# Optimization experiments

Measured on AMD Instinct MI355X. Metric: run time of the kernel, lower is better.

## Reference

```python
import jax, jax.numpy as jnp
import numpy as np

LAYERS = [2, 1024, 512, 256, 128, 1]
LB = jnp.array([0.0, 0.0], dtype=jnp.float32)
UB = jnp.array([2.0 * np.pi, 1.0], dtype=jnp.float32)


def _block_diag_mask(num_blocks, bs1, bs2):
    return jnp.kron(jnp.eye(num_blocks, dtype=jnp.float32), jnp.ones((bs1, bs2), jnp.float32))


def _masks():
    # masks for l in range(2, num_Layers - 2) with num_Layers = len(LAYERS) = 6 -> l in {2, 3}
    width = [LAYERS[0]] + [(2 ** (i - 1)) * LAYERS[i] for i in range(1, len(LAYERS) - 1)] + [LAYERS[-1]]
    masks = []
    for l in range(2, len(LAYERS) - 2):
        num_blocks = 2 ** (l - 1)
        bs1 = width[l] // num_blocks
        bs2 = 2 * LAYERS[l + 1]
        masks.append(_block_diag_mask(num_blocks, bs1, bs2))
    return masks


def setup_inputs() -> dict:
    key = jax.random.key(0)
    ks = jax.random.split(key, 8)
    N = 65536
    H = 1024

    def xavier(k, fi, fo):
        lim = float(np.sqrt(6.0 / (fi + fo)))
        return jax.random.uniform(k, (fi, fo), jnp.float32, -lim, lim)

    X = jax.random.uniform(ks[0], (N, 2), jnp.float32, 0.0, 1.0) * (UB - LB) + LB
    return {
        "X": X,
        "W0": xavier(ks[1], 2, H), "b0": jnp.zeros((1, H), jnp.float32),
        "W1": xavier(ks[2], H, H), "b1": jnp.zeros((1, H), jnp.float32),
        "W2": xavier(ks[3], H, H), "b2": jnp.zeros((1, H), jnp.float32),
        "W3": xavier(ks[4], H, H), "b3": jnp.zeros((1, H), jnp.float32),
        "W_last": xavier(ks[5], H, 1), "b_last": jnp.zeros((1, 1), jnp.float32),
    }


def reference(X, W0, b0, W1, b1, W2, b2, W3, b3, W_last, b_last):
    mask2, mask3 = _masks()
    # input normalization to [-1, 1]
    h = 2.0 * (X - LB) / (UB - LB) - 1.0
    h = jnp.tanh(h @ W0 + b0)                 # layer 0: dense
    h = jnp.tanh(h @ W1 + b1)                 # layer 1: dense (no mask in forward)
    h = jnp.tanh(h @ (W2 * mask2) + b2)       # layer 2: block-diagonal masked
    h = jnp.tanh(h @ (W3 * mask3) + b3)       # layer 3: block-diagonal masked
    return h @ W_last + b_last                # output layer, [N, 1]
```

## Files before the change

kernel.cpp:

```cpp
#include <hip/hip_runtime.h>
#include <cstdint>
#include <cstddef>


typedef _Float16  f16x8   __attribute__((ext_vector_type(8)));
typedef float     floatx4 __attribute__((ext_vector_type(4)));
typedef float     floatx8 __attribute__((ext_vector_type(8)));

__device__ __forceinline__ float tanh_fast(float x) {
    float e = __expf(2.0f * x);
    return 1.0f - 2.0f / (e + 1.0f);
}

__device__ __forceinline__ void gload16(const _Float16* g, _Float16* l) {
    __builtin_amdgcn_global_load_lds(
        (const __attribute__((address_space(1))) unsigned int*)g,
        (__attribute__((address_space(3))) unsigned int*)l, 16, 0, 0);
}

__global__ __launch_bounds__(256)
void transposeH(const float* __restrict__ W, _Float16* __restrict__ Wt) {
    __shared__ float tile[32][33];
    const int tx = threadIdx.x & 31;
    const int ty = threadIdx.x >> 5;
    #pragma unroll
    for (int j = 0; j < 4; ++j) {
        int r = ty + j * 8;
        tile[r][tx] = W[(size_t)(blockIdx.y * 32 + r) * 1024 + blockIdx.x * 32 + tx];
    }
    __syncthreads();
    #pragma unroll
    for (int j = 0; j < 4; ++j) {
        int r = ty + j * 8;
        Wt[(size_t)(blockIdx.x * 32 + r) * 1024 + blockIdx.y * 32 + tx] =
            (_Float16)tile[tx][r];
    }
}

__global__ __launch_bounds__(256)
void init_out(float* __restrict__ out, const float* __restrict__ bl) {
    out[blockIdx.x * 256 + threadIdx.x] = bl[0];
}

__global__ __launch_bounds__(256)
void layer0_kernel(const float* __restrict__ X, const float* __restrict__ W0,
                   const float* __restrict__ b0, _Float16* __restrict__ H) {
    const int idx = blockIdx.x * 256 + threadIdx.x;
    const int row = idx >> 7;
    const int j0  = (idx & 127) << 3;
    const float x0 = X[row * 2 + 0];
    const float x1 = X[row * 2 + 1];
    const float xa = x0 * 0.31830988618379067f - 1.0f;
    const float xb = 2.0f * x1 - 1.0f;
    floatx8 wa = *(const floatx8*)(W0 + j0);
    floatx8 wb = *(const floatx8*)(W0 + 1024 + j0);
    floatx8 bb = *(const floatx8*)(b0 + j0);
    f16x8 o;
    #pragma unroll
    for (int j = 0; j < 8; ++j) {
        float v = fmaf(xa, wa[j], fmaf(xb, wb[j], bb[j]));
        o[j] = (_Float16)tanh_fast(v);
    }
    *(f16x8*)(H + (size_t)row * 1024 + j0) = o;
}

template <bool FUSE>
__global__ __launch_bounds__(512)
void gemm256(const _Float16* __restrict__ A, const _Float16* __restrict__ Bt,
             const float* __restrict__ bias, _Float16* __restrict__ C,
             const float* __restrict__ Wl, float* __restrict__ out, int KB) {
    __shared__ _Float16 As[2 * 8192];
    __shared__ _Float16 Bs[2 * 8192];

    const int tid  = threadIdx.x;
    const int lane = tid & 63;
    const int w    = tid >> 6;

    const int total = gridDim.x * gridDim.y;
    int lid = blockIdx.y * 4 + blockIdx.x;
    if ((total & 7) == 0) {
        const int qq = total >> 3;
        lid = (lid & 7) * qq + (lid >> 3);
    }
    const int n0 = (lid & 3) << 8;
    const int m0 = (lid >> 2) << 8;

    const int kbeg = (n0 / KB) * KB;
    const int NT   = KB >> 5;

    const int c0  = w * 128 + lane;
    const int c1  = c0 + 64;
    const int rw0 = c0 >> 2, sl0 = (c0 & 3) ^ ((rw0 >> 1) & 3);
    const int rw1 = c1 >> 2, sl1 = (c1 & 3) ^ ((rw1 >> 1) & 3);
    const _Float16* gA0 = A  + (size_t)(m0 + rw0) * 1024 + kbeg + sl0 * 8;
    const _Float16* gA1 = A  + (size_t)(m0 + rw1) * 1024 + kbeg + sl1 * 8;
    const _Float16* gB0 = Bt + (size_t)(n0 + rw0) * 1024 + kbeg + sl0 * 8;
    const _Float16* gB1 = Bt + (size_t)(n0 + rw1) * 1024 + kbeg + sl1 * 8;
    const int ldsC0 = c0 * 8, ldsC1 = c1 * 8;

    const int r   = lane & 15, q = lane >> 4;
    const int swz = (q ^ ((r >> 1) & 3)) << 3;
    const int wm  = (w & 1) << 7;
    const int wn  = (w >> 1) << 6;

    floatx4 acc[8][4];
    #pragma unroll
    for (int i = 0; i < 8; ++i)
        #pragma unroll
        for (int j = 0; j < 4; ++j)
            acc[i][j] = floatx4{0.f, 0.f, 0.f, 0.f};

#define STAGE(tt) do {                                        \
        const int _s  = ((tt) & 1) * 8192;                    \
        const int _ko = (tt) * 32;                            \
        gload16(gA0 + _ko, As + _s + ldsC0);                  \
        gload16(gA1 + _ko, As + _s + ldsC1);                  \
        gload16(gB0 + _ko, Bs + _s + ldsC0);                  \
        gload16(gB1 + _ko, Bs + _s + ldsC1);                  \
    } while (0)

    STAGE(0);
    __syncthreads();

    for (int t = 0; t < NT; ++t) {
        if (t + 1 < NT) STAGE(t + 1);

        const _Float16* At = As + (t & 1) * 8192;
        const _Float16* Bw = Bs + (t & 1) * 8192;
        f16x8 af[8], bf[4];
        #pragma unroll
        for (int i = 0; i < 8; ++i)
            af[i] = *(const f16x8*)(At + (wm + i * 16 + r) * 32 + swz);
        #pragma unroll
        for (int j = 0; j < 4; ++j)
            bf[j] = *(const f16x8*)(Bw + (wn + j * 16 + r) * 32 + swz);

        __builtin_amdgcn_s_setprio(1);
        #pragma unroll
        for (int i = 0; i < 8; ++i)
            #pragma unroll
            for (int j = 0; j < 4; ++j)
                acc[i][j] = __builtin_amdgcn_mfma_f32_16x16x32_f16(af[i], bf[j], acc[i][j], 0, 0, 0);
        __builtin_amdgcn_s_setprio(0);

        __syncthreads();
    }
#undef STAGE

    float bv[4], wlv[4];
    #pragma unroll
    for (int j = 0; j < 4; ++j) {
        const int col = n0 + wn + j * 16 + r;
        bv[j] = bias[col];
        if (FUSE) wlv[j] = Wl[col];
    }
    #pragma unroll
    for (int i = 0; i < 8; ++i) {
        const int row0 = m0 + wm + i * 16 + q * 4;
        #pragma unroll
        for (int rr = 0; rr < 4; ++rr) {
            if (!FUSE) {
                #pragma unroll
                for (int j = 0; j < 4; ++j) {
                    float o = tanh_fast(acc[i][j][rr] + bv[j]);
                    const int col = n0 + wn + j * 16 + r;
                    C[(size_t)(row0 + rr) * 1024 + col] = (_Float16)o;
                }
            } else {
                float p = 0.f;
                #pragma unroll
                for (int j = 0; j < 4; ++j)
                    p = fmaf(tanh_fast(acc[i][j][rr] + bv[j]), wlv[j], p);
                p += __shfl_down(p, 8);
                p += __shfl_down(p, 4);
                p += __shfl_down(p, 2);
                p += __shfl_down(p, 1);
                if (r == 0) atomicAdd(out + row0 + rr, p);
            }
        }
    }
}

extern "C" void kernel_launch(void* const* d_in, const int* in_sizes, int n_in,
                              void* d_out, int out_size, void* d_ws, size_t ws_size,
                              hipStream_t stream) {
    const float* X  = (const float*)d_in[0];
    const float* W0 = (const float*)d_in[1];
    const float* b0 = (const float*)d_in[2];
    const float* W1 = (const float*)d_in[3];
    const float* b1 = (const float*)d_in[4];
    const float* W2 = (const float*)d_in[5];
    const float* b2 = (const float*)d_in[6];
    const float* W3 = (const float*)d_in[7];
    const float* b3 = (const float*)d_in[8];
    const float* Wl = (const float*)d_in[9];
    const float* bl = (const float*)d_in[10];
    float* out = (float*)d_out;

    const int Nrows = in_sizes[0] / 2;
    const size_t WT = 1024 * 1024;
    const size_t wt_bytes = 3 * WT * 2;
    const size_t slack = 512;

    int R = 0;
    const int Rcap = Nrows < 32768 ? Nrows : 32768;
    for (int r = Rcap; r >= 256; r >>= 1)
        if ((size_t)2 * r * 2048 + wt_bytes + slack <= ws_size) { R = r; break; }
    if (!R) return;

    _Float16* wsp = (_Float16*)d_ws;
    _Float16* Wt1 = wsp;
    _Float16* Wt2 = Wt1 + WT;
    _Float16* Wt3 = Wt2 + WT;
    const size_t plane = (size_t)R * 1024;
    _Float16* P0 = Wt3 + WT;
    _Float16* P1 = P0 + plane;

    const dim3 tb(256);
    transposeH<<<dim3(32, 32), tb, 0, stream>>>(W1, Wt1);
    transposeH<<<dim3(32, 32), tb, 0, stream>>>(W2, Wt2);
    transposeH<<<dim3(32, 32), tb, 0, stream>>>(W3, Wt3);
    init_out<<<Nrows / 256, tb, 0, stream>>>(out, bl);

    const int nchunks = Nrows / R;
    for (int c = 0; c < nchunks; ++c) {
        const float* Xc = X + (size_t)c * R * 2;
        float* outc = out + (size_t)c * R;

        layer0_kernel<<<R / 2, tb, 0, stream>>>(Xc, W0, b0, P0);

        const dim3 tg(512);
        const dim3 gg(4, R / 256);
        gemm256<false><<<gg, tg, 0, stream>>>(P0, Wt1, b1, P1, nullptr, nullptr, 1024);
        gemm256<false><<<gg, tg, 0, stream>>>(P1, Wt2, b2, P0, nullptr, nullptr, 512);
        gemm256<true ><<<gg, tg, 0, stream>>>(P0, Wt3, b3, nullptr, Wl, outc, 256);
    }
}
```

Measured before the change: 554.5 us.

## Replace 256x256 double-buffered GEMM with simpler 128x128 single-buffered tile

Switches the MFMA GEMM from a 256x256 tile with 512 threads and double-buffered LDS to a 128x128 tile with 256 threads and a single LDS buffer. The block swizzle and priority hints are removed, and loads are now fenced by two barriers per k-step. This lowers LDS and register use per block, which may allow more resident blocks. In exchange it loses global-load/compute overlap and halves data reuse per tile.

```diff
diff --git a/kernel.cpp b/kernel.cpp
--- a/kernel.cpp
+++ b/kernel.cpp
@@ -65,31 +65,25 @@
 }
 
 template <bool FUSE>
-__global__ __launch_bounds__(512)
-void gemm256(const _Float16* __restrict__ A, const _Float16* __restrict__ Bt,
+__global__ __launch_bounds__(256)
+void gemm128(const _Float16* __restrict__ A, const _Float16* __restrict__ Bt,
              const float* __restrict__ bias, _Float16* __restrict__ C,
              const float* __restrict__ Wl, float* __restrict__ out, int KB) {
-    __shared__ _Float16 As[2 * 8192];
-    __shared__ _Float16 Bs[2 * 8192];
+    __shared__ _Float16 As[4096];
+    __shared__ _Float16 Bs[4096];
 
     const int tid  = threadIdx.x;
     const int lane = tid & 63;
     const int w    = tid >> 6;
 
-    const int total = gridDim.x * gridDim.y;
-    int lid = blockIdx.y * 4 + blockIdx.x;
-    if ((total & 7) == 0) {
-        const int qq = total >> 3;
-        lid = (lid & 7) * qq + (lid >> 3);
-    }
-    const int n0 = (lid & 3) << 8;
-    const int m0 = (lid >> 2) << 8;
+    const int m0 = blockIdx.x << 7;
+    const int n0 = blockIdx.y << 7;
 
     const int kbeg = (n0 / KB) * KB;
     const int NT   = KB >> 5;
 
-    const int c0  = w * 128 + lane;
-    const int c1  = c0 + 64;
+    const int c0  = tid;
+    const int c1  = tid + 256;
     const int rw0 = c0 >> 2, sl0 = (c0 & 3) ^ ((rw0 >> 1) & 3);
     const int rw1 = c1 >> 2, sl1 = (c1 & 3) ^ ((rw1 >> 1) & 3);
     const _Float16* gA0 = A  + (size_t)(m0 + rw0) * 1024 + kbeg + sl0 * 8;
@@ -100,50 +94,40 @@
 
     const int r   = lane & 15, q = lane >> 4;
     const int swz = (q ^ ((r >> 1) & 3)) << 3;
-    const int wm  = (w & 1) << 7;
+    const int wm  = (w & 1) << 6;
     const int wn  = (w >> 1) << 6;
 
-    floatx4 acc[8][4];
-    #pragma unroll
-    for (int i = 0; i < 8; ++i)
+    floatx4 acc[4][4];
+    #pragma unroll
+    for (int i = 0; i < 4; ++i)
         #pragma unroll
         for (int j = 0; j < 4; ++j)
             acc[i][j] = floatx4{0.f, 0.f, 0.f, 0.f};
 
 #define STAGE(tt) do {                                        \
-        const int _s  = ((tt) & 1) * 8192;                    \
         const int _ko = (tt) * 32;                            \
-        gload16(gA0 + _ko, As + _s + ldsC0);                  \
-        gload16(gA1 + _ko, As + _s + ldsC1);                  \
-        gload16(gB0 + _ko, Bs + _s + ldsC0);                  \
-        gload16(gB1 + _ko, Bs + _s + ldsC1);                  \
+        gload16(gA0 + _ko, As + ldsC0);                       \
+        gload16(gA1 + _ko, As + ldsC1);                       \
+        gload16(gB0 + _ko, Bs + ldsC0);                       \
+        gload16(gB1 + _ko, Bs + ldsC1);                       \
     } while (0)
 
-    STAGE(0);
-    __syncthreads();
-
     for (int t = 0; t < NT; ++t) {
-        if (t + 1 < NT) STAGE(t + 1);
-
-        const _Float16* At = As + (t & 1) * 8192;
-        const _Float16* Bw = Bs + (t & 1) * 8192;
-        f16x8 af[8], bf[4];
-        #pragma unroll
-        for (int i = 0; i < 8; ++i)
-            af[i] = *(const f16x8*)(At + (wm + i * 16 + r) * 32 + swz);
-        #pragma unroll
-        for (int j = 0; j < 4; ++j)
-            bf[j] = *(const f16x8*)(Bw + (wn + j * 16 + r) * 32 + swz);
-
-        __builtin_amdgcn_s_setprio(1);
-        #pragma unroll
-        for (int i = 0; i < 8; ++i)
+        __syncthreads();
+        STAGE(t);
+        __syncthreads();
+
+        f16x8 af[4], bf[4];
+        #pragma unroll
+        for (int i = 0; i < 4; ++i) {
+            af[i] = *(const f16x8*)(As + (wm + i * 16 + r) * 32 + swz);
+            bf[i] = *(const f16x8*)(Bs + (wn + i * 16 + r) * 32 + swz);
+        }
+        #pragma unroll
+        for (int i = 0; i < 4; ++i)
             #pragma unroll
             for (int j = 0; j < 4; ++j)
                 acc[i][j] = __builtin_amdgcn_mfma_f32_16x16x32_f16(af[i], bf[j], acc[i][j], 0, 0, 0);
-        __builtin_amdgcn_s_setprio(0);
-
-        __syncthreads();
     }
 #undef STAGE
 
@@ -155,7 +139,7 @@
         if (FUSE) wlv[j] = Wl[col];
     }
     #pragma unroll
-    for (int i = 0; i < 8; ++i) {
+    for (int i = 0; i < 4; ++i) {
         const int row0 = m0 + wm + i * 16 + q * 4;
         #pragma unroll
         for (int rr = 0; rr < 4; ++rr) {
@@ -229,10 +213,9 @@
 
         layer0_kernel<<<R / 2, tb, 0, stream>>>(Xc, W0, b0, P0);
 
-        const dim3 tg(512);
-        const dim3 gg(4, R / 256);
-        gemm256<false><<<gg, tg, 0, stream>>>(P0, Wt1, b1, P1, nullptr, nullptr, 1024);
-        gemm256<false><<<gg, tg, 0, stream>>>(P1, Wt2, b2, P0, nullptr, nullptr, 512);
-        gemm256<true ><<<gg, tg, 0, stream>>>(P0, Wt3, b3, nullptr, Wl, outc, 256);
-    }
-}
+        const dim3 gg(R / 128, 8);
+        gemm128<false><<<gg, tb, 0, stream>>>(P0, Wt1, b1, P1, nullptr, nullptr, 1024);
+        gemm128<false><<<gg, tb, 0, stream>>>(P1, Wt2, b2, P0, nullptr, nullptr, 512);
+        gemm128<true ><<<gg, tb, 0, stream>>>(P0, Wt3, b3, nullptr, Wl, outc, 256);
+    }
+}
```

After: 557.7 us. Within noise of the previous version (+0.6%).
